# Kernel tuning notes

Hardware: AMD Instinct MI355X
Metric: run time of the kernel (lower is better)

The kernel has to match this reference:

```python
import jax, jax.numpy as jnp
import numpy as np

LN_EPS = 1e-5


def conv2d(x, w, b, stride, pad):
    # x: NCHW, w: OIHW
    y = jax.lax.conv_general_dilated(
        x, w, (stride, stride), [(pad, pad), (pad, pad)],
        dimension_numbers=("NCHW", "OIHW", "NCHW"))
    return y + b[None, :, None, None]


def gdn(x, gamma, beta):
    # y_c = x_c / sqrt(beta_c + sum_j gamma_cj * x_j^2)  (1x1 conv on x^2)
    norm = jnp.einsum("bchw,dc->bdhw", x * x, gamma) + beta[None, :, None, None]
    return x / jnp.sqrt(norm)


def layernorm(x, w, b):
    mu = jnp.mean(x, axis=-1, keepdims=True)
    var = jnp.var(x, axis=-1, keepdims=True)
    return (x - mu) / jnp.sqrt(var + LN_EPS) * w + b


def setup_inputs() -> dict:
    key = jax.random.key(0)
    ks = jax.random.split(key, 16)
    r = lambda i, shape: (jax.random.normal(ks[i], shape) * 0.02).astype(jnp.float32)
    N, M, K, D = 128, 192, 192, 128
    return {
        "x_p": jax.random.normal(ks[0], (4, 16, 3, 64, 64), jnp.float32),
        "y_g": jax.random.normal(ks[1], (64, K, 32), jnp.float32),
        "conv1_w": r(2, (N, 3, 5, 5)), "conv1_b": jnp.zeros((N,), jnp.float32),
        "gamma1": (0.1 * jnp.eye(N) + 1e-3).astype(jnp.float32), "beta1": jnp.ones((N,), jnp.float32),
        "conv2_w": r(3, (N, N, 5, 5)), "conv2_b": jnp.zeros((N,), jnp.float32),
        "gamma2": (0.1 * jnp.eye(N) + 1e-3).astype(jnp.float32), "beta2": jnp.ones((N,), jnp.float32),
        "conv3_w": r(4, (M, N, 3, 3)), "conv3_b": jnp.zeros((M,), jnp.float32),
        "ln_q_w": jnp.ones((M,), jnp.float32), "ln_q_b": jnp.zeros((M,), jnp.float32),
        "ln_kv_w": jnp.ones((K,), jnp.float32), "ln_kv_b": jnp.zeros((K,), jnp.float32),
        "ln_out_w": jnp.ones((M,), jnp.float32), "ln_out_b": jnp.zeros((M,), jnp.float32),
        "Wq": r(5, (D, M)), "Wk": r(6, (D, K)), "v_w": r(7, (1, D)),
        "Wv": r(8, (M, K)), "out_w": r(9, (M, M)), "out_b": jnp.zeros((M,), jnp.float32),
    }


def reference(x_p, y_g, conv1_w, conv1_b, gamma1, beta1, conv2_w, conv2_b,
              gamma2, beta2, conv3_w, conv3_b, ln_q_w, ln_q_b, ln_kv_w, ln_kv_b,
              ln_out_w, ln_out_b, Wq, Wk, v_w, Wv, out_w, out_b):
    B, P, C, Hp, Wp = x_p.shape
    x = x_p.reshape(B * P, C, Hp, Wp)
    # local encoder: conv s2 -> GDN -> conv s2 -> GDN -> conv s1 k3
    x = gdn(conv2d(x, conv1_w, conv1_b, 2, 2), gamma1, beta1)
    x = gdn(conv2d(x, conv2_w, conv2_b, 2, 2), gamma2, beta2)
    y_local = conv2d(x, conv3_w, conv3_b, 1, 1)          # (BP, M, h, w)
    BP, M, h, w = y_local.shape
    q = y_local.reshape(BP, M, h * w).transpose(0, 2, 1)  # (BP, Tq, M)
    kv = y_g.reshape(BP, y_g.shape[1], -1).transpose(0, 2, 1)  # (BP, Tk, K)
    q = layernorm(q, ln_q_w, ln_q_b)
    kv = layernorm(kv, ln_kv_w, ln_kv_b)
    # Bahdanau additive attention
    q_proj = jnp.einsum("bqm,dm->bqd", q, Wq)            # (BP, Tq, D)
    k_proj = jnp.einsum("bkc,dc->bkd", kv, Wk)           # (BP, Tk, D)
    energy = jnp.einsum("bqkd,d->bqk",
                        jnp.tanh(q_proj[:, :, None, :] + k_proj[:, None, :, :]),
                        v_w[0])                           # (BP, Tq, Tk)
    alpha = jax.nn.softmax(energy, axis=-1)
    v_proj = jnp.einsum("bkc,mc->bkm", kv, Wv)           # (BP, Tk, M)
    context = jnp.einsum("bqk,bkm->bqm", alpha, v_proj)
    context = jnp.einsum("bqm,nm->bqn", context, out_w) + out_b
    fused = layernorm(q + context, ln_out_w, ln_out_b)
    return fused.transpose(0, 2, 1).reshape(BP, M, h, w)
```

## Files before the change

kernel.cpp:

```cpp
#include <hip/hip_runtime.h>
#include <cstddef>
#include <cstdint>


typedef __bf16 bf16x8 __attribute__((ext_vector_type(8)));
typedef float floatx4 __attribute__((ext_vector_type(4)));
typedef unsigned short ushortT;
typedef unsigned short ushort8v __attribute__((ext_vector_type(8)));

#if __has_builtin(__builtin_amdgcn_exp2f)
#define EXP2F(x) __builtin_amdgcn_exp2f(x)
#else
#define EXP2F(x) exp2f(x)
#endif
#if __has_builtin(__builtin_amdgcn_rcpf)
#define RCPF(x) __builtin_amdgcn_rcpf(x)
#else
#define RCPF(x) (1.f / (x))
#endif

__device__ __forceinline__ ushortT f2bf(float f) {
  unsigned u = __builtin_bit_cast(unsigned, f);
  unsigned r = (u + 0x7FFFu + ((u >> 16) & 1u)) >> 16;
  return (ushortT)r;
}
__device__ __forceinline__ float bf2f(ushortT u) {
  return __builtin_bit_cast(float, ((unsigned)u) << 16);
}

static constexpr size_t OFF_T1BF = 0;
static constexpr size_t OFF_X2BF = 4194304;
static constexpr size_t OFF_T2BF = 8388608;
static constexpr size_t OFF_X3BF = 9437184;
static constexpr size_t OFF_QRAW = 10485760;
static constexpr size_t OFF_QLNB = 16777216;
static constexpr size_t OFF_KVB  = 18350080;
static constexpr size_t OFF_QP   = 18546688;
static constexpr size_t OFF_KP   = 20643840;
static constexpr size_t OFF_VP   = 20905984;
static constexpr size_t OFF_WBQ  = 21299200;
static constexpr size_t OFF_WBK  = 21311488;
static constexpr size_t OFF_WBV  = 21323776;
static constexpr size_t OFF_WBO  = 21342208;
static constexpr size_t OFF_CTXB = 21360640;
static constexpr size_t OFF_CTX2 = 22933504;
static constexpr size_t OFF_WT2  = 26079232;
static constexpr size_t OFF_WT3  = 26284032;
static constexpr size_t OFF_WC1  = 26394624;
static constexpr size_t OFF_GB1  = 26406912;
static constexpr size_t OFF_GB2  = 26415104;

__device__ __constant__ int d_TWI2[4][9] = {{ 0, 2, 4,10,12,14,20,22,24},
                                            { 1, 3,11,13,21,23, 0, 0, 0},
                                            { 5, 7, 9,15,17,19, 0, 0, 0},
                                            { 6, 8,16,18, 0, 0, 0, 0, 0}};
__device__ __constant__ int d_NT2[4] = {9, 6, 6, 4};

__device__ void dev_convw3(const float* w, ushortT* wt, int mode, int total,
                           int idx) {
  if (idx >= total) return;
  int j    = idx & 7;
  int om   = (idx >> 3) & 63;
  int kg   = (idx >> 9) & 3;
  int slab = idx >> 11;
  int mt, s, tap, T;
  if (mode == 0) {
    int ph;
    if (slab < 72) ph = 0; else if (slab < 120) ph = 1;
    else if (slab < 168) ph = 2; else ph = 3;
    const int st[4] = {0, 72, 120, 168};
    const int ns[4] = {36, 24, 24, 16};
    int rel = slab - st[ph];
    mt = rel / ns[ph]; s = rel % ns[ph];
    tap = d_TWI2[ph][s >> 2]; T = 25;
  } else {
    mt = slab / 36; s = slab % 36; tap = s >> 2; T = 9;
  }
  int cc = s & 3;
  int c  = cc * 32 + kg * 8 + j;
  int oc = mt * 64 + om;
  wt[idx] = f2bf(w[(size_t)(oc * 128 + c) * T + tap]);
}

__device__ void dev_convw1(const float* w, ushortT* wt, int idx) {
  if (idx >= 20480) return;
  int k    = idx & 31;
  int oc   = (idx >> 5) & 127;
  int slab = idx >> 12;
  int ph, i;
  if (slab < 2) { ph = 0; i = slab; } else { ph = slab - 1; i = 0; }
  int kg = k >> 3, jj = k & 7;
  int tidx = i * 8 + jj;
  float val = 0.f;
  if (kg < 3 && tidx < d_NT2[ph]) {
    int tap = d_TWI2[ph][tidx];
    val = w[(size_t)(oc * 3 + kg) * 25 + tap];
  }
  wt[idx] = f2bf(val);
}

__device__ void dev_wcast(const float* w, ushortT* wb, int total, float scale,
                          int idx) {
  if (idx < total) wb[idx] = f2bf(w[idx] * scale);
}

__global__ __launch_bounds__(256) void prep_kernel(
    const float* __restrict__ conv2_w, ushortT* __restrict__ wt2,
    const float* __restrict__ conv3_w, ushortT* __restrict__ wt3,
    const float* __restrict__ conv1_w, ushortT* __restrict__ wc1,
    const float* __restrict__ Wq, ushortT* __restrict__ wbq,
    const float* __restrict__ Wk, ushortT* __restrict__ wbk,
    const float* __restrict__ Wv, ushortT* __restrict__ wbv,
    const float* __restrict__ out_w, ushortT* __restrict__ wbo,
    const float* __restrict__ gamma1, ushortT* __restrict__ gb1,
    const float* __restrict__ gamma2, ushortT* __restrict__ gb2) {
  constexpr float C2LE = 2.88539008177792681f;
  int blk = blockIdx.x, tid = threadIdx.x;
  if (blk < 1600)      dev_convw3(conv2_w, wt2, 0, 409600, blk * 256 + tid);
  else if (blk < 2464) dev_convw3(conv3_w, wt3, 1, 221184, (blk - 1600) * 256 + tid);
  else if (blk < 2544) dev_convw1(conv1_w, wc1, (blk - 2464) * 256 + tid);
  else if (blk < 2640) dev_wcast(Wq, wbq, 24576, C2LE, (blk - 2544) * 256 + tid);
  else if (blk < 2736) dev_wcast(Wk, wbk, 24576, C2LE, (blk - 2640) * 256 + tid);
  else if (blk < 2880) dev_wcast(Wv, wbv, 36864, 1.f, (blk - 2736) * 256 + tid);
  else if (blk < 3024) dev_wcast(out_w, wbo, 36864, 1.f, (blk - 2880) * 256 + tid);
  else if (blk < 3088) dev_wcast(gamma1, gb1, 16384, 1.f, (blk - 3024) * 256 + tid);
  else                 dev_wcast(gamma2, gb2, 16384, 1.f, (blk - 3088) * 256 + tid);
}

__global__ __launch_bounds__(256, 1) void conv1_mfma_kernel(
    const float* __restrict__ x, const ushortT* __restrict__ wc1,
    const float* __restrict__ bias, ushortT* __restrict__ outb) {
  int b  = blockIdx.x >> 2;
  int yg = blockIdx.x & 3;
  int y0 = yg * 8;

  int wave = threadIdx.x >> 6;
  int lane = threadIdx.x & 63;
  int ln15 = lane & 15;
  int kg   = lane >> 4;
  int tid  = threadIdx.x;

  __shared__ ushortT simg[4680];
  __shared__ ushortT sA[5 * 128 * 40];

  for (int j = tid; j < 2340; j += 256) ((unsigned*)simg)[j] = 0u;
  __syncthreads();

  int ihBase = 2 * y0 - 2;
  const float* xb = x + (size_t)b * 3 * 4096;
  for (int j = tid; j < 960; j += 256) {
    int q = j & 15;
    int rr = j >> 4;
    int c = rr / 20, ihl = rr % 20;
    int ih = ihBase + ihl;
    if (ih >= 0 && ih < 64) {
      float4 v = *(const float4*)&xb[c * 4096 + ih * 64 + q * 4];
      int pr = ih & 1, u = ih >> 1;
      int lr = u - y0 + 1;
      int base0 = ((pr * 2 + 0) * 3 + c) * 360 + lr * 36;
      int base1 = ((pr * 2 + 1) * 3 + c) * 360 + lr * 36;
      simg[base0 + 2 * q + 1] = f2bf(v.x);
      simg[base1 + 2 * q + 1] = f2bf(v.y);
      simg[base0 + 2 * q + 2] = f2bf(v.z);
      simg[base1 + 2 * q + 2] = f2bf(v.w);
    }
  }
  for (int j = tid; j < 2560; j += 256) {
    int chunk = j & 3, row = j >> 2;
    uint4 v = *(const uint4*)&wc1[row * 32 + chunk * 8];
    *(uint4*)&sA[row * 40 + chunk * 8] = v;
  }
  __syncthreads();

  constexpr int TDR[4][9] = {{-1,-1,-1, 0, 0, 0, 1, 1, 1},
                             {-1,-1, 0, 0, 1, 1, 0, 0, 0},
                             {-1,-1,-1, 0, 0, 0, 0, 0, 0},
                             {-1,-1, 0, 0, 0, 0, 0, 0, 0}};
  constexpr int TDC[4][9] = {{-1, 0, 1,-1, 0, 1,-1, 0, 1},
                             {-1, 0,-1, 0,-1, 0, 0, 0, 0},
                             {-1, 0, 1,-1, 0, 1, 0, 0, 0},
                             {-1, 0,-1, 0, 0, 0, 0, 0, 0}};
  constexpr int NT[4]  = {9, 6, 6, 4};
  constexpr int NM[4]  = {2, 1, 1, 1};
  constexpr int SB[4]  = {0, 2, 3, 4};

  ushort8v Bf[4][5];
  #pragma unroll
  for (int ntl = 0; ntl < 4; ++ntl) {
    int ntg = wave * 4 + ntl;
    int yloc = ntg >> 1;
    int xx = (ntg & 1) * 16 + ln15;
    int lbase = (yloc + 1) * 36 + xx + 1 + kg * 360;
    #pragma unroll
    for (int ph = 0; ph < 4; ++ph) {
      int pbase = ph * 1080 + lbase;
      #pragma unroll
      for (int i = 0; i < 2; ++i) {
        if (i < NM[ph]) {
          ushort8v bv;
          #pragma unroll
          for (int j = 0; j < 8; ++j) {
            int tidx = i * 8 + j;
            if (tidx >= NT[ph]) tidx = 0;
            int off = TDR[ph][tidx] * 36 + TDC[ph][tidx];
            bv[j] = simg[pbase + off];
          }
          Bf[ntl][SB[ph] + i] = bv;
        }
      }
    }
  }

  #pragma unroll
  for (int m = 0; m < 8; ++m) {
    bf16x8 Af[5];
    #pragma unroll
    for (int s = 0; s < 5; ++s)
      Af[s] = *(const bf16x8*)&sA[(s * 128 + m * 16 + ln15) * 40 + kg * 8];
    int oc0 = m * 16 + kg * 4;
    float4 bv = *(const float4*)&bias[oc0];
    #pragma unroll
    for (int ntl = 0; ntl < 4; ++ntl) {
      floatx4 acc = (floatx4)0.f;
      #pragma unroll
      for (int s = 0; s < 5; ++s)
        acc = __builtin_amdgcn_mfma_f32_16x16x32_bf16(
            Af[s], __builtin_bit_cast(bf16x8, Bf[ntl][s]), acc, 0, 0, 0);
      int ntg = wave * 4 + ntl;
      int y = y0 + (ntg >> 1);
      int xx = (ntg & 1) * 16 + ln15;
      int p = y * 32 + xx;
      ushort4 o4 = {f2bf(acc[0] + bv.x), f2bf(acc[1] + bv.y),
                    f2bf(acc[2] + bv.z), f2bf(acc[3] + bv.w)};
      *(ushort4*)&outb[((size_t)b * 1024 + p) * 128 + oc0] = o4;
    }
  }
}

__global__ __launch_bounds__(256) void gdn_mfma_kernel(
    const ushortT* __restrict__ xbf, const ushortT* __restrict__ gb,
    const float* __restrict__ beta, ushortT* __restrict__ ybf,
    int HW, int nPixTiles, int isSplit) {
  int pt = blockIdx.x % nPixTiles;
  int b  = blockIdx.x / nPixTiles;
  int px0 = pt * 64;
  int tid = threadIdx.x;
  int wave = tid >> 6, lane = tid & 63, ln15 = lane & 15, kg = lane >> 4;

  __shared__ ushortT sG[128 * 136];
  __shared__ ushortT sX[64 * 136];

  for (int j = tid; j < 2048; j += 256) {
    int row = j >> 4, ch = j & 15;
    *(uint4*)&sG[row * 136 + ch * 8] = *(const uint4*)&gb[row * 128 + ch * 8];
  }
  for (int j = tid; j < 1024; j += 256) {
    int row = j >> 4, ch = j & 15;
    ushort8v xv = *(const ushort8v*)&xbf[((size_t)(b * HW + px0 + row)) * 128 + ch * 8];
    ushort8v sq;
    #pragma unroll
    for (int r = 0; r < 8; ++r) {
      float f = bf2f(xv[r]);
      sq[r] = f2bf(f * f);
    }
    *(ushort8v*)&sX[row * 136 + ch * 8] = sq;
  }
  __syncthreads();

  floatx4 acc[2][4];
  #pragma unroll
  for (int mi = 0; mi < 2; ++mi)
    #pragma unroll
    for (int nt = 0; nt < 4; ++nt) acc[mi][nt] = (floatx4)0.f;

  #pragma unroll
  for (int k0 = 0; k0 < 128; k0 += 32) {
    bf16x8 a0 = *(const bf16x8*)&sG[(wave * 32 + ln15) * 136 + k0 + kg * 8];
    bf16x8 a1 = *(const bf16x8*)&sG[(wave * 32 + 16 + ln15) * 136 + k0 + kg * 8];
    #pragma unroll
    for (int nt = 0; nt < 4; ++nt) {
      bf16x8 bb = *(const bf16x8*)&sX[(nt * 16 + ln15) * 136 + k0 + kg * 8];
      acc[0][nt] = __builtin_amdgcn_mfma_f32_16x16x32_bf16(a0, bb, acc[0][nt], 0, 0, 0);
      acc[1][nt] = __builtin_amdgcn_mfma_f32_16x16x32_bf16(a1, bb, acc[1][nt], 0, 0, 0);
    }
  }

  #pragma unroll
  for (int mi = 0; mi < 2; ++mi) {
    int d0 = wave * 32 + mi * 16 + kg * 4;
    float4 bt = *(const float4*)&beta[d0];
    #pragma unroll
    for (int nt = 0; nt < 4; ++nt) {
      int p = px0 + nt * 16 + ln15;
      ushort4 x4 = *(const ushort4*)&xbf[((size_t)(b * HW + p)) * 128 + d0];
      ushort4 o4;
      o4.x = f2bf(bf2f(x4.x) * rsqrtf(acc[mi][nt][0] + bt.x));
      o4.y = f2bf(bf2f(x4.y) * rsqrtf(acc[mi][nt][1] + bt.y));
      o4.z = f2bf(bf2f(x4.z) * rsqrtf(acc[mi][nt][2] + bt.z));
      o4.w = f2bf(bf2f(x4.w) * rsqrtf(acc[mi][nt][3] + bt.w));
      size_t dst;
      if (isSplit) {
        int h = p >> 5, w5 = p & 31;
        int ph = ((h & 1) << 1) | (w5 & 1);
        dst = (((size_t)b * 4 + ph) * 256 + (h >> 1) * 16 + (w5 >> 1)) * 128 + d0;
      } else {
        dst = ((size_t)b * 256 + p) * 128 + d0;
      }
      *(ushort4*)&ybf[dst] = o4;
    }
  }
}

template<int MODE>
__global__ __launch_bounds__(256, 2) void conv_mfma_kernel(
    const ushortT* __restrict__ X,
    const ushortT* __restrict__ Wt,
    const float* __restrict__ bias,
    ushortT* __restrict__ outb, float* __restrict__ outf) {
  constexpr int OC  = (MODE == 0) ? 128 : 192;
  constexpr int NMT = OC / 64;
  constexpr int NPH = (MODE == 0) ? 4 : 1;

  int b   = blockIdx.x / (NMT * 4);
  int rem = blockIdx.x % (NMT * 4);
  int mt  = rem >> 2;
  int rs  = rem & 3;
  int r0  = rs * 4;

  int wave = threadIdx.x >> 6;
  int lane = threadIdx.x & 63;
  int ln15 = lane & 15;
  int kg   = lane >> 4;

  __shared__ ushortT simg[6 * 18 * 136];

  floatx4 acc[4];
  #pragma unroll
  for (int m = 0; m < 4; ++m) acc[m] = (floatx4)0.f;

  constexpr int NS2[4]      = {36, 24, 24, 16};
  constexpr int PHSTART2[4] = {0, 72, 120, 168};
  constexpr int TDR_2[4][9] = {{-1,-1,-1, 0, 0, 0, 1, 1, 1},
                               {-1,-1, 0, 0, 1, 1, 0, 0, 0},
                               {-1,-1,-1, 0, 0, 0, 0, 0, 0},
                               {-1,-1, 0, 0, 0, 0, 0, 0, 0}};
  constexpr int TDC_2[4][9] = {{-1, 0, 1,-1, 0, 1,-1, 0, 1},
                               {-1, 0,-1, 0,-1, 0, 0, 0, 0},
                               {-1, 0, 1,-1, 0, 1, 0, 0, 0},
                               {-1, 0,-1, 0, 0, 0, 0, 0, 0}};
  constexpr int TDR_3[9] = {-1,-1,-1, 0, 0, 0, 1, 1, 1};
  constexpr int TDC_3[9] = {-1, 0, 1,-1, 0, 1,-1, 0, 1};

  const int aoff = kg * 512 + ln15 * 8;
  uint4 apf[8][4];

  #pragma unroll
  for (int ph = 0; ph < NPH; ++ph) {
    const int NS = (MODE == 0) ? NS2[ph] : 36;
    const int slabBase = (MODE == 0) ? (PHSTART2[ph] + mt * NS2[ph]) : (mt * 36);
    const ushortT* wp0 = Wt + (size_t)slabBase * 2048 + aoff;

    __syncthreads();
    const ushortT* Xb = X + (((size_t)b * NPH + ph) * 256) * 128;
    for (int idx = threadIdx.x; idx < 1728; idx += 256) {
      int chunk = idx & 15;
      int pix = idx >> 4;
      int row = pix / 18, colm = pix - row * 18;
      int i = r0 - 1 + row, j = colm - 1;
      uint4 v = {0u, 0u, 0u, 0u};
      if (i >= 0 && i < 16 && j >= 0 && j < 16)
        v = *(const uint4*)(Xb + ((size_t)(i * 16 + j)) * 128 + chunk * 8);
      *(uint4*)&simg[(row * 18 + colm) * 136 + chunk * 8] = v;
    }
    #pragma unroll
    for (int jj = 0; jj < 8; ++jj)
      if (jj < NS) {
        #pragma unroll
        for (int m = 0; m < 4; ++m)
          apf[jj][m] = *(const uint4*)(wp0 + (size_t)jj * 2048 + m * 128);
      }
    __syncthreads();

    #pragma unroll
    for (int s0 = 0; s0 < NS; s0 += 8) {
      #pragma unroll
      for (int jj = 0; jj < 8; ++jj) {
        int s = s0 + jj;
        if (s < NS) {
          bf16x8 acur[4];
          #pragma unroll
          for (int m = 0; m < 4; ++m) acur[m] = __builtin_bit_cast(bf16x8, apf[jj][m]);
          int sp = s + 8;
          if (sp < NS) {
            #pragma unroll
            for (int m = 0; m < 4; ++m)
              apf[jj][m] = *(const uint4*)(wp0 + (size_t)sp * 2048 + m * 128);
          }
          int t  = s >> 2;
          int c0 = (s & 3) * 32;
          int dr = (MODE == 0) ? TDR_2[ph][t] : TDR_3[t];
          int dc = (MODE == 0) ? TDC_2[ph][t] : TDC_3[t];
          int lrow = wave + dr + 1;
          int lcol = ln15 + dc + 1;
          bf16x8 bfr = *(const bf16x8*)&simg[(lrow * 18 + lcol) * 136 + c0 + kg * 8];
          #pragma unroll
          for (int m = 0; m < 4; ++m)
            acc[m] = __builtin_amdgcn_mfma_f32_16x16x32_bf16(acur[m], bfr, acc[m], 0, 0, 0);
        }
      }
    }
  }

  #pragma unroll
  for (int m = 0; m < 4; ++m) {
    int mg = mt * 64 + m * 16 + kg * 4;
    float4 bv = *(const float4*)&bias[mg];
    int r = r0 + wave;
    int p = r * 16 + ln15;
    if (MODE == 0) {
      ushort4 o4 = {f2bf(acc[m][0] + bv.x), f2bf(acc[m][1] + bv.y),
                    f2bf(acc[m][2] + bv.z), f2bf(acc[m][3] + bv.w)};
      *(ushort4*)&outb[((size_t)b * 256 + p) * 128 + mg] = o4;
    } else {
      float4 o4 = {acc[m][0] + bv.x, acc[m][1] + bv.y,
                   acc[m][2] + bv.z, acc[m][3] + bv.w};
      *(float4*)&outf[((size_t)b * 256 + p) * OC + mg] = o4;
    }
  }
}

__device__ __forceinline__ void gemm_body(
    const ushortT* A, const ushortT* Bm, const float* bias, float* C,
    int N, int r0, int n0, int tid) {
  __shared__ ushortT sA[128 * 196];
  __shared__ ushortT sB[64 * 196];
  for (int j = tid; j < 3072; j += 256) {
    int row = j / 24, ch = j % 24;
    *(ushort8v*)&sA[row * 196 + ch * 8] = *(const ushort8v*)&A[(size_t)(r0 + row) * 192 + ch * 8];
  }
  for (int j = tid; j < 1536; j += 256) {
    int row = j / 24, ch = j % 24;
    *(ushort8v*)&sB[row * 196 + ch * 8] = *(const ushort8v*)&Bm[(size_t)(n0 + row) * 192 + ch * 8];
  }
  __syncthreads();
  int wave = tid >> 6, lane = tid & 63, ln15 = lane & 15, kg = lane >> 4;
  floatx4 acc[2][4];
  #pragma unroll
  for (int m = 0; m < 2; ++m)
    #pragma unroll
    for (int n = 0; n < 4; ++n) acc[m][n] = (floatx4)0.f;

  #pragma unroll
  for (int k0 = 0; k0 < 192; k0 += 32) {
    bf16x8 afr[2];
    #pragma unroll
    for (int m = 0; m < 2; ++m)
      afr[m] = *(const bf16x8*)&sA[(wave * 32 + m * 16 + ln15) * 196 + k0 + kg * 8];
    #pragma unroll
    for (int n = 0; n < 4; ++n) {
      bf16x8 bfr = *(const bf16x8*)&sB[(n * 16 + ln15) * 196 + k0 + kg * 8];
      acc[0][n] = __builtin_amdgcn_mfma_f32_16x16x32_bf16(afr[0], bfr, acc[0][n], 0, 0, 0);
      acc[1][n] = __builtin_amdgcn_mfma_f32_16x16x32_bf16(afr[1], bfr, acc[1][n], 0, 0, 0);
    }
  }
  #pragma unroll
  for (int n = 0; n < 4; ++n) {
    int col = n0 + n * 16 + ln15;
    float bv = bias ? bias[col] : 0.f;
    #pragma unroll
    for (int m = 0; m < 2; ++m) {
      int rowb = r0 + wave * 32 + m * 16 + kg * 4;
      #pragma unroll
      for (int r = 0; r < 4; ++r)
        C[(size_t)(rowb + r) * N + col] = acc[m][n][r] + bv;
    }
  }
}

__global__ __launch_bounds__(256) void gemm_qkv_kernel(
    const ushortT* __restrict__ qlnb, const ushortT* __restrict__ kvb,
    const ushortT* __restrict__ wbq, const ushortT* __restrict__ wbk,
    const ushortT* __restrict__ wbv,
    float* __restrict__ qproj, float* __restrict__ kproj,
    float* __restrict__ vproj) {
  int blk = blockIdx.x, tid = threadIdx.x;
  if (blk < 256) {
    gemm_body(qlnb, wbq, nullptr, qproj, 128, (blk >> 1) * 128, (blk & 1) * 64, tid);
  } else if (blk < 288) {
    int k = blk - 256;
    gemm_body(kvb, wbk, nullptr, kproj, 128, (k >> 1) * 128, (k & 1) * 64, tid);
  } else {
    int k = blk - 288;
    gemm_body(kvb, wbv, nullptr, vproj, 192, (k / 3) * 128, (k % 3) * 64, tid);
  }
}

__global__ __launch_bounds__(256) void gemm_out_kernel(
    const ushortT* __restrict__ A, const ushortT* __restrict__ Bm,
    const float* __restrict__ bias, float* __restrict__ C) {
  gemm_body(A, Bm, bias, C, 192, (blockIdx.x / 3) * 128, (blockIdx.x % 3) * 64,
            threadIdx.x);
}

__global__ __launch_bounds__(256) void ln_all_kernel(
    const float* __restrict__ qraw, const float* __restrict__ qw,
    const float* __restrict__ qb, ushortT* __restrict__ qlnb,
    const float* __restrict__ yg, const float* __restrict__ kw,
    const float* __restrict__ kb, ushortT* __restrict__ kvb) {
  int lane = threadIdx.x & 63;
  if (blockIdx.x < 4096) {
    int row = blockIdx.x * 4 + (threadIdx.x >> 6);
    const float* xr = qraw + (size_t)row * 192;
    float v0 = xr[lane], v1 = xr[lane + 64], v2 = xr[lane + 128];
    float s = v0 + v1 + v2;
    float s2 = v0 * v0 + v1 * v1 + v2 * v2;
    #pragma unroll
    for (int off = 32; off; off >>= 1) { s += __shfl_xor(s, off); s2 += __shfl_xor(s2, off); }
    float mean = s * (1.f / 192.f);
    float var = s2 * (1.f / 192.f) - mean * mean;
    float inv = rsqrtf(var + 1e-5f);
    ushortT* ybr = qlnb + (size_t)row * 192;
    ybr[lane]       = f2bf((v0 - mean) * inv * qw[lane]       + qb[lane]);
    ybr[lane + 64]  = f2bf((v1 - mean) * inv * qw[lane + 64]  + qb[lane + 64]);
    ybr[lane + 128] = f2bf((v2 - mean) * inv * qw[lane + 128] + qb[lane + 128]);
  } else {
    int row = (blockIdx.x - 4096) * 4 + (threadIdx.x >> 6);
    int b = row >> 5, t = row & 31;
    const float* src = yg + (size_t)b * 6144 + t;
    float v0 = src[(size_t)lane * 32];
    float v1 = src[(size_t)(lane + 64) * 32];
    float v2 = src[(size_t)(lane + 128) * 32];
    float s = v0 + v1 + v2;
    float s2 = v0 * v0 + v1 * v1 + v2 * v2;
    #pragma unroll
    for (int off = 32; off; off >>= 1) { s += __shfl_xor(s, off); s2 += __shfl_xor(s2, off); }
    float mean = s * (1.f / 192.f);
    float var = s2 * (1.f / 192.f) - mean * mean;
    float inv = rsqrtf(var + 1e-5f);
    ushortT* yr = kvb + (size_t)row * 192;
    yr[lane]       = f2bf((v0 - mean) * inv * kw[lane]       + kb[lane]);
    yr[lane + 64]  = f2bf((v1 - mean) * inv * kw[lane + 64]  + kb[lane + 64]);
    yr[lane + 128] = f2bf((v2 - mean) * inv * kw[lane + 128] + kb[lane + 128]);
  }
}

__global__ __launch_bounds__(256) void attn_kernel(
    const float* __restrict__ qp, const float* __restrict__ kp,
    const float* __restrict__ vp, const float* __restrict__ vw,
    ushortT* __restrict__ ctxb) {
  int b = blockIdx.x >> 4;
  int q0 = (blockIdx.x & 15) * 16;
  __shared__ float skp[32 * 132];
  __shared__ float sqp[16 * 132];
  __shared__ float svp[32 * 192];
  __shared__ float se[16][33];
  __shared__ float swm[128];
  __shared__ float sS0;
  int tid = threadIdx.x;

  const float4* kp4 = (const float4*)(kp + (size_t)b * 32 * 128);
  for (int j = tid; j < 32 * 32; j += 256) {
    int k = j >> 5, d4 = j & 31;
    float4 v = kp4[k * 32 + d4];
    *(float4*)&skp[k * 132 + d4 * 4] = v;
  }
  const float4* qp4 = (const float4*)(qp + (size_t)(b * 256 + q0) * 128);
  for (int j = tid; j < 16 * 32; j += 256) {
    int qq = j >> 5, d4 = j & 31;
    float4 v = qp4[qq * 32 + d4];
    *(float4*)&sqp[qq * 132 + d4 * 4] = v;
  }
  const float4* vp4 = (const float4*)(vp + (size_t)b * 32 * 192);
  for (int j = tid; j < 32 * 48; j += 256) {
    int k = j / 48, m4 = j % 48;
    *(float4*)&svp[k * 192 + m4 * 4] = vp4[k * 48 + m4];
  }
  if (tid < 128) swm[tid] = -2.f * vw[tid];
  if (tid < 64) {
    float s = vw[tid] + vw[tid + 64];
    #pragma unroll
    for (int off = 32; off; off >>= 1) s += __shfl_xor(s, off);
    if (tid == 0) sS0 = s;
  }
  __syncthreads();

  {
    int qq = tid >> 4, kc = tid & 15;
    const float4* q4 = (const float4*)&sqp[qq * 132];
    const float4* ka = (const float4*)&skp[kc * 132];
    const float4* kb = (const float4*)&skp[(kc + 16) * 132];
    const float4* w4 = (const float4*)swm;
    float S0 = sS0;
    float acc0 = S0, acc1 = S0;
    #pragma unroll 8
    for (int dj = 0; dj < 32; ++dj) {
      float4 qv = q4[dj], k0 = ka[dj], k1 = kb[dj], wv = w4[dj];
      acc0 += wv.x * RCPF(EXP2F(qv.x + k0.x) + 1.f);
      acc0 += wv.y * RCPF(EXP2F(qv.y + k0.y) + 1.f);
      acc0 += wv.z * RCPF(EXP2F(qv.z + k0.z) + 1.f);
      acc0 += wv.w * RCPF(EXP2F(qv.w + k0.w) + 1.f);
      acc1 += wv.x * RCPF(EXP2F(qv.x + k1.x) + 1.f);
      acc1 += wv.y * RCPF(EXP2F(qv.y + k1.y) + 1.f);
      acc1 += wv.z * RCPF(EXP2F(qv.z + k1.z) + 1.f);
      acc1 += wv.w * RCPF(EXP2F(qv.w + k1.w) + 1.f);
    }
    se[qq][kc] = acc0;
    se[qq][kc + 16] = acc1;
  }
  __syncthreads();
  if (tid < 16) {
    float mx = -1e30f;
    for (int k = 0; k < 32; ++k) mx = fmaxf(mx, se[tid][k]);
    float s = 0.f;
    for (int k = 0; k < 32; ++k) { float a = __expf(se[tid][k] - mx); se[tid][k] = a; s += a; }
    float invs = 1.f / s;
    for (int k = 0; k < 32; ++k) se[tid][k] *= invs;
  }
  __syncthreads();
  for (int j = tid; j < 768; j += 256) {
    int qq = j / 48, m4 = j % 48;
    const float* al = se[qq];
    float4 a = {0.f, 0.f, 0.f, 0.f};
    #pragma unroll 8
    for (int k = 0; k < 32; ++k) {
      float wk = al[k];
      float4 v = *(const float4*)&svp[k * 192 + m4 * 4];
      a.x += wk * v.x; a.y += wk * v.y; a.z += wk * v.z; a.w += wk * v.w;
    }
    ushort4 o4 = {f2bf(a.x), f2bf(a.y), f2bf(a.z), f2bf(a.w)};
    *(ushort4*)&ctxb[((size_t)(b * 256 + q0 + qq)) * 192 + m4 * 4] = o4;
  }
}

__global__ __launch_bounds__(256) void lnout_kernel(
    const ushortT* __restrict__ qlnb, const float* __restrict__ ctx2,
    const float* __restrict__ w, const float* __restrict__ bb,
    float* __restrict__ out) {
  int b = blockIdx.x >> 2;
  int t0 = (blockIdx.x & 3) * 64;
  __shared__ float sf[64 * 193];
  int wid = threadIdx.x >> 6, lane = threadIdx.x & 63;
  for (int rr = wid; rr < 64; rr += 4) {
    size_t base = ((size_t)(b * 256 + t0 + rr)) * 192;
    float v0 = bf2f(qlnb[base + lane])       + ctx2[base + lane];
    float v1 = bf2f(qlnb[base + lane + 64])  + ctx2[base + lane + 64];
    float v2 = bf2f(qlnb[base + lane + 128]) + ctx2[base + lane + 128];
    float s = v0 + v1 + v2;
    float s2 = v0 * v0 + v1 * v1 + v2 * v2;
    #pragma unroll
    for (int off = 32; off; off >>= 1) { s += __shfl_xor(s, off); s2 += __shfl_xor(s2, off); }
    float mean = s * (1.f / 192.f);
    float var = s2 * (1.f / 192.f) - mean * mean;
    float inv = rsqrtf(var + 1e-5f);
    sf[rr * 193 + lane]       = (v0 - mean) * inv * w[lane]       + bb[lane];
    sf[rr * 193 + lane + 64]  = (v1 - mean) * inv * w[lane + 64]  + bb[lane + 64];
    sf[rr * 193 + lane + 128] = (v2 - mean) * inv * w[lane + 128] + bb[lane + 128];
  }
  __syncthreads();
  for (int j = threadIdx.x; j < 192 * 16; j += 256) {
    int m = j >> 4, t4 = j & 15;
    float4 o4;
    o4.x = sf[(t4 * 4 + 0) * 193 + m];
    o4.y = sf[(t4 * 4 + 1) * 193 + m];
    o4.z = sf[(t4 * 4 + 2) * 193 + m];
    o4.w = sf[(t4 * 4 + 3) * 193 + m];
    *(float4*)&out[((size_t)(b * 192 + m)) * 256 + t0 + t4 * 4] = o4;
  }
}

extern "C" void kernel_launch(void* const* d_in, const int* in_sizes, int n_in,
                              void* d_out, int out_size, void* d_ws, size_t ws_size,
                              hipStream_t stream) {
  (void)in_sizes; (void)n_in; (void)out_size; (void)ws_size;
  const float* x_p     = (const float*)d_in[0];
  const float* y_g     = (const float*)d_in[1];
  const float* conv1_w = (const float*)d_in[2];
  const float* conv1_b = (const float*)d_in[3];
  const float* gamma1  = (const float*)d_in[4];
  const float* beta1   = (const float*)d_in[5];
  const float* conv2_w = (const float*)d_in[6];
  const float* conv2_b = (const float*)d_in[7];
  const float* gamma2  = (const float*)d_in[8];
  const float* beta2   = (const float*)d_in[9];
  const float* conv3_w = (const float*)d_in[10];
  const float* conv3_b = (const float*)d_in[11];
  const float* ln_q_w  = (const float*)d_in[12];
  const float* ln_q_b  = (const float*)d_in[13];
  const float* ln_kv_w = (const float*)d_in[14];
  const float* ln_kv_b = (const float*)d_in[15];
  const float* ln_out_w= (const float*)d_in[16];
  const float* ln_out_b= (const float*)d_in[17];
  const float* Wq      = (const float*)d_in[18];
  const float* Wk      = (const float*)d_in[19];
  const float* v_w     = (const float*)d_in[20];
  const float* Wv      = (const float*)d_in[21];
  const float* out_w   = (const float*)d_in[22];
  const float* out_b   = (const float*)d_in[23];
  float* out = (float*)d_out;
  float* ws  = (float*)d_ws;

  ushortT* t1bf  = (ushortT*)(ws + OFF_T1BF);
  ushortT* x2bf  = (ushortT*)(ws + OFF_X2BF);
  ushortT* t2bf  = (ushortT*)(ws + OFF_T2BF);
  ushortT* x3bf  = (ushortT*)(ws + OFF_X3BF);
  float*   qraw  = ws + OFF_QRAW;
  ushortT* qlnb  = (ushortT*)(ws + OFF_QLNB);
  ushortT* kvb   = (ushortT*)(ws + OFF_KVB);
  float*   qproj = ws + OFF_QP;
  float*   kproj = ws + OFF_KP;
  float*   vproj = ws + OFF_VP;
  ushortT* wbq   = (ushortT*)(ws + OFF_WBQ);
  ushortT* wbk   = (ushortT*)(ws + OFF_WBK);
  ushortT* wbv   = (ushortT*)(ws + OFF_WBV);
  ushortT* wbo   = (ushortT*)(ws + OFF_WBO);
  ushortT* ctxb  = (ushortT*)(ws + OFF_CTXB);
  float*   ctx2  = ws + OFF_CTX2;
  ushortT* wt2   = (ushortT*)(ws + OFF_WT2);
  ushortT* wt3   = (ushortT*)(ws + OFF_WT3);
  ushortT* wc1   = (ushortT*)(ws + OFF_WC1);
  ushortT* gb1   = (ushortT*)(ws + OFF_GB1);
  ushortT* gb2   = (ushortT*)(ws + OFF_GB2);

  prep_kernel<<<3152, 256, 0, stream>>>(conv2_w, wt2, conv3_w, wt3, conv1_w, wc1,
                                        Wq, wbq, Wk, wbk, Wv, wbv, out_w, wbo,
                                        gamma1, gb1, gamma2, gb2);
  conv1_mfma_kernel<<<256, 256, 0, stream>>>(x_p, wc1, conv1_b, t1bf);
  gdn_mfma_kernel<<<1024, 256, 0, stream>>>(t1bf, gb1, beta1, x2bf, 1024, 16, 1);
  conv_mfma_kernel<0><<<512, 256, 0, stream>>>(x2bf, wt2, conv2_b, t2bf, nullptr);
  gdn_mfma_kernel<<<256, 256, 0, stream>>>(t2bf, gb2, beta2, x3bf, 256, 4, 0);
  conv_mfma_kernel<1><<<768, 256, 0, stream>>>(x3bf, wt3, conv3_b, nullptr, qraw);
  ln_all_kernel<<<4608, 256, 0, stream>>>(qraw, ln_q_w, ln_q_b, qlnb,
                                          y_g, ln_kv_w, ln_kv_b, kvb);
  gemm_qkv_kernel<<<336, 256, 0, stream>>>(qlnb, kvb, wbq, wbk, wbv,
                                           qproj, kproj, vproj);
  attn_kernel<<<1024, 256, 0, stream>>>(qproj, kproj, vproj, v_w, ctxb);
  gemm_out_kernel<<<384, 256, 0, stream>>>(ctxb, wbo, out_b, ctx2);
  lnout_kernel<<<256, 256, 0, stream>>>(qlnb, ctx2, ln_out_w, ln_out_b, out);
}
```

Measured before the change: 261.0 us.

## Store intermediates in bf16 and fuse output projection into final layernorm

The conv3 output and the q/k/v projection results are now stored as bf16 instead of fp32, which halves their global memory traffic. The attention kernel converts them back to float when loading into shared memory. The separate output-projection GEMM is folded into the final layernorm kernel, which computes the MFMA product straight into shared memory and so drops one launch and the fp32 ctx2 round trip. This lowers precision on q_proj, k_proj and v_proj and on the pre-layernorm activations. The fused kernel also reads A and B fragments directly from global memory without staging them in shared memory.

New measurement: 264.1 us. About the same (+1.2%).

```diff
diff --git a/kernel.cpp b/kernel.cpp
--- a/kernel.cpp
+++ b/kernel.cpp
@@ -43,7 +43,6 @@
 static constexpr size_t OFF_WBV  = 21323776;
 static constexpr size_t OFF_WBO  = 21342208;
 static constexpr size_t OFF_CTXB = 21360640;
-static constexpr size_t OFF_CTX2 = 22933504;
 static constexpr size_t OFF_WT2  = 26079232;
 static constexpr size_t OFF_WT3  = 26284032;
 static constexpr size_t OFF_WC1  = 26394624;
@@ -316,7 +315,7 @@
     const ushortT* __restrict__ X,
     const ushortT* __restrict__ Wt,
     const float* __restrict__ bias,
-    ushortT* __restrict__ outb, float* __restrict__ outf) {
+    ushortT* __restrict__ outb) {
   constexpr int OC  = (MODE == 0) ? 128 : 192;
   constexpr int NMT = OC / 64;
   constexpr int NPH = (MODE == 0) ? 4 : 1;
@@ -417,20 +416,14 @@
     float4 bv = *(const float4*)&bias[mg];
     int r = r0 + wave;
     int p = r * 16 + ln15;
-    if (MODE == 0) {
-      ushort4 o4 = {f2bf(acc[m][0] + bv.x), f2bf(acc[m][1] + bv.y),
-                    f2bf(acc[m][2] + bv.z), f2bf(acc[m][3] + bv.w)};
-      *(ushort4*)&outb[((size_t)b * 256 + p) * 128 + mg] = o4;
-    } else {
-      float4 o4 = {acc[m][0] + bv.x, acc[m][1] + bv.y,
-                   acc[m][2] + bv.z, acc[m][3] + bv.w};
-      *(float4*)&outf[((size_t)b * 256 + p) * OC + mg] = o4;
-    }
+    ushort4 o4 = {f2bf(acc[m][0] + bv.x), f2bf(acc[m][1] + bv.y),
+                  f2bf(acc[m][2] + bv.z), f2bf(acc[m][3] + bv.w)};
+    *(ushort4*)&outb[((size_t)b * 256 + p) * OC + mg] = o4;
   }
 }
 
 __device__ __forceinline__ void gemm_body(
-    const ushortT* A, const ushortT* Bm, const float* bias, float* C,
+    const ushortT* A, const ushortT* Bm, ushortT* C,
     int N, int r0, int n0, int tid) {
   __shared__ ushortT sA[128 * 196];
   __shared__ ushortT sB[64 * 196];
@@ -466,13 +459,12 @@
   #pragma unroll
   for (int n = 0; n < 4; ++n) {
     int col = n0 + n * 16 + ln15;
-    float bv = bias ? bias[col] : 0.f;
     #pragma unroll
     for (int m = 0; m < 2; ++m) {
       int rowb = r0 + wave * 32 + m * 16 + kg * 4;
       #pragma unroll
       for (int r = 0; r < 4; ++r)
-        C[(size_t)(rowb + r) * N + col] = acc[m][n][r] + bv;
+        C[(size_t)(rowb + r) * N + col] = f2bf(acc[m][n][r]);
     }
   }
 }
@@ -481,37 +473,30 @@
     const ushortT* __restrict__ qlnb, const ushortT* __restrict__ kvb,
     const ushortT* __restrict__ wbq, const ushortT* __restrict__ wbk,
     const ushortT* __restrict__ wbv,
-    float* __restrict__ qproj, float* __restrict__ kproj,
-    float* __restrict__ vproj) {
+    ushortT* __restrict__ qpb, ushortT* __restrict__ kpb,
+    ushortT* __restrict__ vpb) {
   int blk = blockIdx.x, tid = threadIdx.x;
   if (blk < 256) {
-    gemm_body(qlnb, wbq, nullptr, qproj, 128, (blk >> 1) * 128, (blk & 1) * 64, tid);
+    gemm_body(qlnb, wbq, qpb, 128, (blk >> 1) * 128, (blk & 1) * 64, tid);
   } else if (blk < 288) {
     int k = blk - 256;
-    gemm_body(kvb, wbk, nullptr, kproj, 128, (k >> 1) * 128, (k & 1) * 64, tid);
+    gemm_body(kvb, wbk, kpb, 128, (k >> 1) * 128, (k & 1) * 64, tid);
   } else {
     int k = blk - 288;
-    gemm_body(kvb, wbv, nullptr, vproj, 192, (k / 3) * 128, (k % 3) * 64, tid);
-  }
-}
-
-__global__ __launch_bounds__(256) void gemm_out_kernel(
-    const ushortT* __restrict__ A, const ushortT* __restrict__ Bm,
-    const float* __restrict__ bias, float* __restrict__ C) {
-  gemm_body(A, Bm, bias, C, 192, (blockIdx.x / 3) * 128, (blockIdx.x % 3) * 64,
-            threadIdx.x);
+    gemm_body(kvb, wbv, vpb, 192, (k / 3) * 128, (k % 3) * 64, tid);
+  }
 }
 
 __global__ __launch_bounds__(256) void ln_all_kernel(
-    const float* __restrict__ qraw, const float* __restrict__ qw,
+    const ushortT* __restrict__ qrawb, const float* __restrict__ qw,
     const float* __restrict__ qb, ushortT* __restrict__ qlnb,
     const float* __restrict__ yg, const float* __restrict__ kw,
     const float* __restrict__ kb, ushortT* __restrict__ kvb) {
   int lane = threadIdx.x & 63;
   if (blockIdx.x < 4096) {
     int row = blockIdx.x * 4 + (threadIdx.x >> 6);
-    const float* xr = qraw + (size_t)row * 192;
-    float v0 = xr[lane], v1 = xr[lane + 64], v2 = xr[lane + 128];
+    const ushortT* xr = qrawb + (size_t)row * 192;
+    float v0 = bf2f(xr[lane]), v1 = bf2f(xr[lane + 64]), v2 = bf2f(xr[lane + 128]);
     float s = v0 + v1 + v2;
     float s2 = v0 * v0 + v1 * v1 + v2 * v2;
     #pragma unroll
@@ -545,8 +530,8 @@
 }
 
 __global__ __launch_bounds__(256) void attn_kernel(
-    const float* __restrict__ qp, const float* __restrict__ kp,
-    const float* __restrict__ vp, const float* __restrict__ vw,
+    const ushortT* __restrict__ qpb, const ushortT* __restrict__ kpb,
+    const ushortT* __restrict__ vpb, const float* __restrict__ vw,
     ushortT* __restrict__ ctxb) {
   int b = blockIdx.x >> 4;
   int q0 = (blockIdx.x & 15) * 16;
@@ -558,22 +543,23 @@
   __shared__ float sS0;
   int tid = threadIdx.x;
 
-  const float4* kp4 = (const float4*)(kp + (size_t)b * 32 * 128);
-  for (int j = tid; j < 32 * 32; j += 256) {
-    int k = j >> 5, d4 = j & 31;
-    float4 v = kp4[k * 32 + d4];
-    *(float4*)&skp[k * 132 + d4 * 4] = v;
-  }
-  const float4* qp4 = (const float4*)(qp + (size_t)(b * 256 + q0) * 128);
-  for (int j = tid; j < 16 * 32; j += 256) {
-    int qq = j >> 5, d4 = j & 31;
-    float4 v = qp4[qq * 32 + d4];
-    *(float4*)&sqp[qq * 132 + d4 * 4] = v;
-  }
-  const float4* vp4 = (const float4*)(vp + (size_t)b * 32 * 192);
-  for (int j = tid; j < 32 * 48; j += 256) {
-    int k = j / 48, m4 = j % 48;
-    *(float4*)&svp[k * 192 + m4 * 4] = vp4[k * 48 + m4];
+  for (int j = tid; j < 512; j += 256) {
+    int k = j >> 4, d8 = j & 15;
+    ushort8v v = *(const ushort8v*)&kpb[((size_t)(b * 32 + k)) * 128 + d8 * 8];
+    #pragma unroll
+    for (int r = 0; r < 8; ++r) skp[k * 132 + d8 * 8 + r] = bf2f(v[r]);
+  }
+  for (int j = tid; j < 256; j += 256) {
+    int qq = j >> 4, d8 = j & 15;
+    ushort8v v = *(const ushort8v*)&qpb[((size_t)(b * 256 + q0 + qq)) * 128 + d8 * 8];
+    #pragma unroll
+    for (int r = 0; r < 8; ++r) sqp[qq * 132 + d8 * 8 + r] = bf2f(v[r]);
+  }
+  for (int j = tid; j < 768; j += 256) {
+    int k = j / 24, c8 = j % 24;
+    ushort8v v = *(const ushort8v*)&vpb[((size_t)(b * 32 + k)) * 192 + c8 * 8];
+    #pragma unroll
+    for (int r = 0; r < 8; ++r) svp[k * 192 + c8 * 8 + r] = bf2f(v[r]);
   }
   if (tid < 128) swm[tid] = -2.f * vw[tid];
   if (tid < 64) {
@@ -632,19 +618,49 @@
   }
 }
 
-__global__ __launch_bounds__(256) void lnout_kernel(
-    const ushortT* __restrict__ qlnb, const float* __restrict__ ctx2,
+__global__ __launch_bounds__(256) void outproj_ln_kernel(
+    const ushortT* __restrict__ ctxb, const ushortT* __restrict__ wbo,
+    const float* __restrict__ out_b, const ushortT* __restrict__ qlnb,
     const float* __restrict__ w, const float* __restrict__ bb,
     float* __restrict__ out) {
   int b = blockIdx.x >> 2;
   int t0 = (blockIdx.x & 3) * 64;
   __shared__ float sf[64 * 193];
-  int wid = threadIdx.x >> 6, lane = threadIdx.x & 63;
-  for (int rr = wid; rr < 64; rr += 4) {
-    size_t base = ((size_t)(b * 256 + t0 + rr)) * 192;
-    float v0 = bf2f(qlnb[base + lane])       + ctx2[base + lane];
-    float v1 = bf2f(qlnb[base + lane + 64])  + ctx2[base + lane + 64];
-    float v2 = bf2f(qlnb[base + lane + 128]) + ctx2[base + lane + 128];
+  int tid = threadIdx.x;
+  int wave = tid >> 6, lane = tid & 63, ln15 = lane & 15, kg = lane >> 4;
+
+  const ushortT* Arow = ctxb + ((size_t)(b * 256 + t0)) * 192;
+
+  #pragma unroll
+  for (int nc = 0; nc < 3; ++nc) {
+    floatx4 acc[4];
+    #pragma unroll
+    for (int n = 0; n < 4; ++n) acc[n] = (floatx4)0.f;
+    #pragma unroll
+    for (int k0 = 0; k0 < 192; k0 += 32) {
+      bf16x8 afr = *(const bf16x8*)&Arow[((size_t)(wave * 16 + ln15)) * 192 + k0 + kg * 8];
+      #pragma unroll
+      for (int n = 0; n < 4; ++n) {
+        bf16x8 bfr = *(const bf16x8*)&wbo[((size_t)(nc * 64 + n * 16 + ln15)) * 192 + k0 + kg * 8];
+        acc[n] = __builtin_amdgcn_mfma_f32_16x16x32_bf16(afr, bfr, acc[n], 0, 0, 0);
+      }
+    }
+    #pragma unroll
+    for (int n = 0; n < 4; ++n) {
+      int col = nc * 64 + n * 16 + ln15;
+      float bv = out_b[col];
+      #pragma unroll
+      for (int r = 0; r < 4; ++r)
+        sf[(wave * 16 + kg * 4 + r) * 193 + col] = acc[n][r] + bv;
+    }
+  }
+  __syncthreads();
+
+  for (int rr = wave; rr < 64; rr += 4) {
+    size_t gb = ((size_t)(b * 256 + t0 + rr)) * 192;
+    float v0 = sf[rr * 193 + lane]       + bf2f(qlnb[gb + lane]);
+    float v1 = sf[rr * 193 + lane + 64]  + bf2f(qlnb[gb + lane + 64]);
+    float v2 = sf[rr * 193 + lane + 128] + bf2f(qlnb[gb + lane + 128]);
     float s = v0 + v1 + v2;
     float s2 = v0 * v0 + v1 * v1 + v2 * v2;
     #pragma unroll
@@ -657,7 +673,8 @@
     sf[rr * 193 + lane + 128] = (v2 - mean) * inv * w[lane + 128] + bb[lane + 128];
   }
   __syncthreads();
-  for (int j = threadIdx.x; j < 192 * 16; j += 256) {
+
+  for (int j = tid; j < 192 * 16; j += 256) {
     int m = j >> 4, t4 = j & 15;
     float4 o4;
     o4.x = sf[(t4 * 4 + 0) * 193 + m];
@@ -703,18 +720,17 @@
   ushortT* x2bf  = (ushortT*)(ws + OFF_X2BF);
   ushortT* t2bf  = (ushortT*)(ws + OFF_T2BF);
   ushortT* x3bf  = (ushortT*)(ws + OFF_X3BF);
-  float*   qraw  = ws + OFF_QRAW;
+  ushortT* qrawb = (ushortT*)(ws + OFF_QRAW);
   ushortT* qlnb  = (ushortT*)(ws + OFF_QLNB);
   ushortT* kvb   = (ushortT*)(ws + OFF_KVB);
-  float*   qproj = ws + OFF_QP;
-  float*   kproj = ws + OFF_KP;
-  float*   vproj = ws + OFF_VP;
+  ushortT* qpb   = (ushortT*)(ws + OFF_QP);
+  ushortT* kpb   = (ushortT*)(ws + OFF_KP);
+  ushortT* vpb   = (ushortT*)(ws + OFF_VP);
   ushortT* wbq   = (ushortT*)(ws + OFF_WBQ);
   ushortT* wbk   = (ushortT*)(ws + OFF_WBK);
   ushortT* wbv   = (ushortT*)(ws + OFF_WBV);
   ushortT* wbo   = (ushortT*)(ws + OFF_WBO);
   ushortT* ctxb  = (ushortT*)(ws + OFF_CTXB);
-  float*   ctx2  = ws + OFF_CTX2;
   ushortT* wt2   = (ushortT*)(ws + OFF_WT2);
   ushortT* wt3   = (ushortT*)(ws + OFF_WT3);
   ushortT* wc1   = (ushortT*)(ws + OFF_WC1);
@@ -726,14 +742,14 @@
                                         gamma1, gb1, gamma2, gb2);
   conv1_mfma_kernel<<<256, 256, 0, stream>>>(x_p, wc1, conv1_b, t1bf);
   gdn_mfma_kernel<<<1024, 256, 0, stream>>>(t1bf, gb1, beta1, x2bf, 1024, 16, 1);
-  conv_mfma_kernel<0><<<512, 256, 0, stream>>>(x2bf, wt2, conv2_b, t2bf, nullptr);
+  conv_mfma_kernel<0><<<512, 256, 0, stream>>>(x2bf, wt2, conv2_b, t2bf);
   gdn_mfma_kernel<<<256, 256, 0, stream>>>(t2bf, gb2, beta2, x3bf, 256, 4, 0);
-  conv_mfma_kernel<1><<<768, 256, 0, stream>>>(x3bf, wt3, conv3_b, nullptr, qraw);
-  ln_all_kernel<<<4608, 256, 0, stream>>>(qraw, ln_q_w, ln_q_b, qlnb,
+  conv_mfma_kernel<1><<<768, 256, 0, stream>>>(x3bf, wt3, conv3_b, qrawb);
+  ln_all_kernel<<<4608, 256, 0, stream>>>(qrawb, ln_q_w, ln_q_b, qlnb,
                                           y_g, ln_kv_w, ln_kv_b, kvb);
   gemm_qkv_kernel<<<336, 256, 0, stream>>>(qlnb, kvb, wbq, wbk, wbv,
-                                           qproj, kproj, vproj);
-  attn_kernel<<<1024, 256, 0, stream>>>(qproj, kproj, vproj, v_w, ctxb);
-  gemm_out_kernel<<<384, 256, 0, stream>>>(ctxb, wbo, out_b, ctx2);
-  lnout_kernel<<<256, 256, 0, stream>>>(qlnb, ctx2, ln_out_w, ln_out_b, out);
-}
+                                           qpb, kpb, vpb);
+  attn_kernel<<<1024, 256, 0, stream>>>(qpb, kpb, vpb, v_w, ctxb);
+  outproj_ln_kernel<<<256, 256, 0, stream>>>(ctxb, wbo, out_b, qlnb,
+                                             ln_out_w, ln_out_b, out);
+}
```
